# Kernel tuning notes

Hardware: AMD Instinct MI355X
Metric: run time of the kernel (lower is better)

## Reference

```python
import jax, jax.numpy as jnp
import numpy as np

B, HQ, HKV, D, S, MB = 64, 32, 8, 128, 16, 128  # batch, q heads, kv heads, head_dim, block_size, max blocks
SCALE = 0.08838834764831845  # 1/sqrt(128)


def setup_inputs() -> dict:
    key = jax.random.key(0)
    k1, k2, k3, k4 = jax.random.split(key, 4)
    num_blocks = B * MB
    q = jax.random.normal(k1, (B, HQ, D), dtype=jnp.float32)
    k_cache = jax.random.normal(k2, (num_blocks, S, HKV, D), dtype=jnp.float32)
    v_cache = jax.random.normal(k3, (num_blocks, S, HKV, D), dtype=jnp.float32)
    block_tables = jnp.arange(num_blocks, dtype=jnp.int32).reshape(B, MB)
    context_lens = jax.random.randint(k4, (B,), 1, S * MB + 1, dtype=jnp.int32)
    return {"q": q, "k_cache": k_cache, "v_cache": v_cache,
            "block_tables": block_tables, "context_lens": context_lens}


def reference(q, k_cache, v_cache, block_tables, context_lens):
    # Paged GQA decode attention: gather KV blocks per request, masked softmax.
    b, hq, d = q.shape
    s, hkv = k_cache.shape[1], k_cache.shape[2]
    g = hq // hkv
    # gather paged KV: [B, MB, S, HKV, D] -> [B, L, HKV, D]
    k = k_cache[block_tables].reshape(b, -1, hkv, d)
    v = v_cache[block_tables].reshape(b, -1, hkv, d)
    L = k.shape[1]
    qg = (q * SCALE).reshape(b, hkv, g, d)  # group query heads per kv head
    scores = jnp.einsum('bhgd,blhd->bhgl', qg, k)
    valid = jnp.arange(L, dtype=jnp.int32)[None, :] < context_lens[:, None]  # [B, L]
    scores = jnp.where(valid[:, None, None, :], scores, -jnp.inf)
    p = jax.nn.softmax(scores, axis=-1)
    o = jnp.einsum('bhgl,blhd->bhgd', p, v).reshape(b, hq, d)
    return o
```

## Files before the change

kernel.cpp:

```cpp
#include <hip/hip_runtime.h>
#include <cstddef>

#define NB    64
#define NHQ   32
#define NHKV  8
#define HD    128
#define BS    16
#define NMB   128
#define NG    4
#define LMAX  2048
#define QK_SCALE 0.08838834764831845f

__global__ __launch_bounds__(256)
void paged_gqa_decode(const float* __restrict__ q,
                      const float* __restrict__ k_cache,
                      const float* __restrict__ v_cache,
                      const int*   __restrict__ block_tables,
                      const int*   __restrict__ context_lens,
                      float* __restrict__ out)
{
    const int bh   = blockIdx.x;
    const int b    = bh >> 3;
    const int h    = bh & 7;
    const int tid  = threadIdx.x;
    const int team = tid >> 5;
    const int lane = tid & 31;

    __shared__ float s_p[LMAX * 4];
    __shared__ float s_acc[8][NG][HD];
    __shared__ int   s_bt[NMB];
    __shared__ float s_l[NG];

    const int len = context_lens[b];

    for (int i = tid; i < NMB; i += 256) s_bt[i] = block_tables[b * NMB + i];

    const float* qb = q + ((size_t)b * NHQ + (size_t)h * NG) * HD + lane * 4;
    float4 q0 = *(const float4*)(qb);
    float4 q1 = *(const float4*)(qb + HD);
    float4 q2 = *(const float4*)(qb + 2 * HD);
    float4 q3 = *(const float4*)(qb + 3 * HD);
    q0.x *= QK_SCALE; q0.y *= QK_SCALE; q0.z *= QK_SCALE; q0.w *= QK_SCALE;
    q1.x *= QK_SCALE; q1.y *= QK_SCALE; q1.z *= QK_SCALE; q1.w *= QK_SCALE;
    q2.x *= QK_SCALE; q2.y *= QK_SCALE; q2.z *= QK_SCALE; q2.w *= QK_SCALE;
    q3.x *= QK_SCALE; q3.y *= QK_SCALE; q3.z *= QK_SCALE; q3.w *= QK_SCALE;

    __syncthreads();

    const float* kbase = k_cache + (size_t)h * HD + lane * 4;
    const float* vbase = v_cache + (size_t)h * HD + lane * 4;

    auto slot_off = [&](int p) -> size_t {
        return (size_t)(s_bt[p >> 4] * BS + (p & 15)) * (NHKV * HD);
    };

    auto qk_one = [&](int p, float4 k4) {
        float d0 = q0.x * k4.x + q0.y * k4.y + q0.z * k4.z + q0.w * k4.w;
        float d1 = q1.x * k4.x + q1.y * k4.y + q1.z * k4.z + q1.w * k4.w;
        float d2 = q2.x * k4.x + q2.y * k4.y + q2.z * k4.z + q2.w * k4.w;
        float d3 = q3.x * k4.x + q3.y * k4.y + q3.z * k4.z + q3.w * k4.w;
#pragma unroll
        for (int off = 16; off >= 1; off >>= 1) {
            d0 += __shfl_xor(d0, off, 32);
            d1 += __shfl_xor(d1, off, 32);
            d2 += __shfl_xor(d2, off, 32);
            d3 += __shfl_xor(d3, off, 32);
        }
        if (lane == 0) {
            float* sp = s_p + 4 * p;
            sp[0] = d0; sp[1] = d1; sp[2] = d2; sp[3] = d3;
        }
    };

    {
        int p = team;
        for (; p + 24 < len; p += 32) {
            float4 k0 = *(const float4*)(kbase + slot_off(p));
            float4 k1 = *(const float4*)(kbase + slot_off(p + 8));
            float4 k2 = *(const float4*)(kbase + slot_off(p + 16));
            float4 k3 = *(const float4*)(kbase + slot_off(p + 24));
            qk_one(p,      k0);
            qk_one(p + 8,  k1);
            qk_one(p + 16, k2);
            qk_one(p + 24, k3);
        }
        for (; p < len; p += 8) {
            float4 k0 = *(const float4*)(kbase + slot_off(p));
            qk_one(p, k0);
        }
    }
    __syncthreads();

    {
        const int wv = tid >> 6;
        const int wl = tid & 63;
        float m = -INFINITY;
        for (int p = wl; p < len; p += 64) m = fmaxf(m, s_p[4 * p + wv]);
#pragma unroll
        for (int off = 32; off >= 1; off >>= 1) m = fmaxf(m, __shfl_xor(m, off, 64));
        float l = 0.0f;
        for (int p = wl; p < len; p += 64) {
            float e = __expf(s_p[4 * p + wv] - m);
            s_p[4 * p + wv] = e;
            l += e;
        }
#pragma unroll
        for (int off = 32; off >= 1; off >>= 1) l += __shfl_xor(l, off, 64);
        if (wl == 0) s_l[wv] = l;
    }
    __syncthreads();

    float4 a0 = make_float4(0.f, 0.f, 0.f, 0.f);
    float4 a1 = a0, a2 = a0, a3 = a0;

    auto pv_one = [&](int p, float4 v4) {
        const float* sp = s_p + 4 * p;
        float w0 = sp[0], w1 = sp[1], w2 = sp[2], w3 = sp[3];
        a0.x += w0 * v4.x; a0.y += w0 * v4.y; a0.z += w0 * v4.z; a0.w += w0 * v4.w;
        a1.x += w1 * v4.x; a1.y += w1 * v4.y; a1.z += w1 * v4.z; a1.w += w1 * v4.w;
        a2.x += w2 * v4.x; a2.y += w2 * v4.y; a2.z += w2 * v4.z; a2.w += w2 * v4.w;
        a3.x += w3 * v4.x; a3.y += w3 * v4.y; a3.z += w3 * v4.z; a3.w += w3 * v4.w;
    };

    {
        int p = team;
        for (; p + 24 < len; p += 32) {
            float4 v0 = *(const float4*)(vbase + slot_off(p));
            float4 v1 = *(const float4*)(vbase + slot_off(p + 8));
            float4 v2 = *(const float4*)(vbase + slot_off(p + 16));
            float4 v3 = *(const float4*)(vbase + slot_off(p + 24));
            pv_one(p,      v0);
            pv_one(p + 8,  v1);
            pv_one(p + 16, v2);
            pv_one(p + 24, v3);
        }
        for (; p < len; p += 8) {
            float4 v0 = *(const float4*)(vbase + slot_off(p));
            pv_one(p, v0);
        }
    }

    *(float4*)&s_acc[team][0][lane * 4] = a0;
    *(float4*)&s_acc[team][1][lane * 4] = a1;
    *(float4*)&s_acc[team][2][lane * 4] = a2;
    *(float4*)&s_acc[team][3][lane * 4] = a3;
    __syncthreads();

    if (tid < 128) {
        const int j = tid >> 5;
        const int c = (tid & 31) << 2;
        float sx = 0.f, sy = 0.f, sz = 0.f, sw = 0.f;
#pragma unroll
        for (int t = 0; t < 8; ++t) {
            const float* a = &s_acc[t][j][c];
            sx += a[0]; sy += a[1]; sz += a[2]; sw += a[3];
        }
        const float inv = 1.0f / s_l[j];
        float4 o = make_float4(sx * inv, sy * inv, sz * inv, sw * inv);
        *(float4*)(out + ((size_t)b * NHQ + (size_t)h * NG + j) * HD + c) = o;
    }
}

extern "C" void kernel_launch(void* const* d_in, const int* in_sizes, int n_in,
                              void* d_out, int out_size, void* d_ws, size_t ws_size,
                              hipStream_t stream) {
    const float* q            = (const float*)d_in[0];
    const float* k_cache      = (const float*)d_in[1];
    const float* v_cache      = (const float*)d_in[2];
    const int*   block_tables = (const int*)d_in[3];
    const int*   context_lens = (const int*)d_in[4];
    float*       out          = (float*)d_out;

    paged_gqa_decode<<<dim3(NB * NHKV), dim3(256), 0, stream>>>(
        q, k_cache, v_cache, block_tables, context_lens, out);
}
```

Before: 911.9 us.

## Split paged attention into sequence chunks with a separate reduction kernel

Splits each (batch, kv-head) decode into four 512-token chunks, each computed by its own workgroup that writes a partial max, sum and unnormalized output to workspace. A second kernel merges the partials with log-sum-exp rescaling. This raises the number of workgroups from 512 to 2048 to fill the GPU better and shrinks shared memory per block, which allows higher occupancy. It also unrolls the K/V loads to 8 per iteration and replaces the full per-query shuffle reduction with a transposed butterfly, at the cost of an extra launch and workspace traffic.

```diff
diff --git a/kernel.cpp b/kernel.cpp
--- a/kernel.cpp
+++ b/kernel.cpp
@@ -1,39 +1,46 @@
 #include <hip/hip_runtime.h>
 #include <cstddef>
 
-#define NB    64
-#define NHQ   32
-#define NHKV  8
-#define HD    128
-#define BS    16
-#define NMB   128
-#define NG    4
-#define LMAX  2048
+#define NB     64
+#define NHQ    32
+#define NHKV   8
+#define HD     128
+#define BS     16
+#define NMB    128
+#define NG     4
+#define CHUNK  512
+#define NCHUNK 4
 #define QK_SCALE 0.08838834764831845f
-
-__global__ __launch_bounds__(256)
-void paged_gqa_decode(const float* __restrict__ q,
-                      const float* __restrict__ k_cache,
-                      const float* __restrict__ v_cache,
-                      const int*   __restrict__ block_tables,
-                      const int*   __restrict__ context_lens,
-                      float* __restrict__ out)
+#define WS_STRIDE 520
+
+__global__ __launch_bounds__(256, 4)
+void pa_partial(const float* __restrict__ q,
+                const float* __restrict__ k_cache,
+                const float* __restrict__ v_cache,
+                const int*   __restrict__ block_tables,
+                const int*   __restrict__ context_lens,
+                float*       __restrict__ ws)
 {
-    const int bh   = blockIdx.x;
-    const int b    = bh >> 3;
-    const int h    = bh & 7;
+    const int c   = blockIdx.x & (NCHUNK - 1);
+    const int bh  = blockIdx.x >> 2;
+    const int b   = bh >> 3;
+    const int h   = bh & 7;
+    const int len = context_lens[b];
+    const int start = c * CHUNK;
+    if (start >= len) return;
+    const int n = min(len - start, CHUNK);
+
     const int tid  = threadIdx.x;
     const int team = tid >> 5;
     const int lane = tid & 31;
 
-    __shared__ float s_p[LMAX * 4];
-    __shared__ float s_acc[8][NG][HD];
-    __shared__ int   s_bt[NMB];
-    __shared__ float s_l[NG];
-
-    const int len = context_lens[b];
-
-    for (int i = tid; i < NMB; i += 256) s_bt[i] = block_tables[b * NMB + i];
+    __shared__ float smem[8 * NG * HD];
+    __shared__ int   s_bt[CHUNK / BS];
+    __shared__ float s_m[NG], s_l[NG];
+
+    float* s_p = smem;
+
+    if (tid < CHUNK / BS) s_bt[tid] = block_tables[b * NMB + (start >> 4) + tid];
 
     const float* qb = q + ((size_t)b * NHQ + (size_t)h * NG) * HD + lane * 4;
     float4 q0 = *(const float4*)(qb);
@@ -50,43 +57,41 @@
     const float* kbase = k_cache + (size_t)h * HD + lane * 4;
     const float* vbase = v_cache + (size_t)h * HD + lane * 4;
 
-    auto slot_off = [&](int p) -> size_t {
-        return (size_t)(s_bt[p >> 4] * BS + (p & 15)) * (NHKV * HD);
+    auto soff = [&](int p) -> size_t {
+        return ((size_t)s_bt[p >> 4] * BS + (size_t)(p & 15)) * (NHKV * HD);
     };
+
+    const bool l1 = (lane & 1) != 0;
+    const bool l2 = (lane & 2) != 0;
 
     auto qk_one = [&](int p, float4 k4) {
         float d0 = q0.x * k4.x + q0.y * k4.y + q0.z * k4.z + q0.w * k4.w;
         float d1 = q1.x * k4.x + q1.y * k4.y + q1.z * k4.z + q1.w * k4.w;
         float d2 = q2.x * k4.x + q2.y * k4.y + q2.z * k4.z + q2.w * k4.w;
         float d3 = q3.x * k4.x + q3.y * k4.y + q3.z * k4.z + q3.w * k4.w;
-#pragma unroll
-        for (int off = 16; off >= 1; off >>= 1) {
-            d0 += __shfl_xor(d0, off, 32);
-            d1 += __shfl_xor(d1, off, 32);
-            d2 += __shfl_xor(d2, off, 32);
-            d3 += __shfl_xor(d3, off, 32);
-        }
-        if (lane == 0) {
-            float* sp = s_p + 4 * p;
-            sp[0] = d0; sp[1] = d1; sp[2] = d2; sp[3] = d3;
-        }
+        float u  = l1 ? d1 : d0, uw = l1 ? d0 : d1;
+        u += __shfl_xor(uw, 1, 32);
+        float v  = l1 ? d3 : d2, vw = l1 ? d2 : d3;
+        v += __shfl_xor(vw, 1, 32);
+        float x  = l2 ? v : u,  y  = l2 ? u : v;
+        x += __shfl_xor(y, 2, 32);
+        x += __shfl_xor(x, 4, 32);
+        x += __shfl_xor(x, 8, 32);
+        x += __shfl_xor(x, 16, 32);
+        if (lane < 4) s_p[4 * p + lane] = x;
     };
 
     {
         int p = team;
-        for (; p + 24 < len; p += 32) {
-            float4 k0 = *(const float4*)(kbase + slot_off(p));
-            float4 k1 = *(const float4*)(kbase + slot_off(p + 8));
-            float4 k2 = *(const float4*)(kbase + slot_off(p + 16));
-            float4 k3 = *(const float4*)(kbase + slot_off(p + 24));
-            qk_one(p,      k0);
-            qk_one(p + 8,  k1);
-            qk_one(p + 16, k2);
-            qk_one(p + 24, k3);
-        }
-        for (; p < len; p += 8) {
-            float4 k0 = *(const float4*)(kbase + slot_off(p));
-            qk_one(p, k0);
+        for (; p + 56 < n; p += 64) {
+            float4 kk[8];
+#pragma unroll
+            for (int u = 0; u < 8; ++u) kk[u] = *(const float4*)(kbase + soff(p + 8 * u));
+#pragma unroll
+            for (int u = 0; u < 8; ++u) qk_one(p + 8 * u, kk[u]);
+        }
+        for (; p < n; p += 8) {
+            qk_one(p, *(const float4*)(kbase + soff(p)));
         }
     }
     __syncthreads();
@@ -95,18 +100,18 @@
         const int wv = tid >> 6;
         const int wl = tid & 63;
         float m = -INFINITY;
-        for (int p = wl; p < len; p += 64) m = fmaxf(m, s_p[4 * p + wv]);
+        for (int p = wl; p < n; p += 64) m = fmaxf(m, s_p[4 * p + wv]);
 #pragma unroll
         for (int off = 32; off >= 1; off >>= 1) m = fmaxf(m, __shfl_xor(m, off, 64));
         float l = 0.0f;
-        for (int p = wl; p < len; p += 64) {
+        for (int p = wl; p < n; p += 64) {
             float e = __expf(s_p[4 * p + wv] - m);
             s_p[4 * p + wv] = e;
             l += e;
         }
 #pragma unroll
         for (int off = 32; off >= 1; off >>= 1) l += __shfl_xor(l, off, 64);
-        if (wl == 0) s_l[wv] = l;
+        if (wl == 0) { s_m[wv] = m; s_l[wv] = l; }
     }
     __syncthreads();
 
@@ -124,40 +129,64 @@
 
     {
         int p = team;
-        for (; p + 24 < len; p += 32) {
-            float4 v0 = *(const float4*)(vbase + slot_off(p));
-            float4 v1 = *(const float4*)(vbase + slot_off(p + 8));
-            float4 v2 = *(const float4*)(vbase + slot_off(p + 16));
-            float4 v3 = *(const float4*)(vbase + slot_off(p + 24));
-            pv_one(p,      v0);
-            pv_one(p + 8,  v1);
-            pv_one(p + 16, v2);
-            pv_one(p + 24, v3);
-        }
-        for (; p < len; p += 8) {
-            float4 v0 = *(const float4*)(vbase + slot_off(p));
-            pv_one(p, v0);
-        }
-    }
-
+        for (; p + 56 < n; p += 64) {
+            float4 vv[8];
+#pragma unroll
+            for (int u = 0; u < 8; ++u) vv[u] = *(const float4*)(vbase + soff(p + 8 * u));
+#pragma unroll
+            for (int u = 0; u < 8; ++u) pv_one(p + 8 * u, vv[u]);
+        }
+        for (; p < n; p += 8) {
+            pv_one(p, *(const float4*)(vbase + soff(p)));
+        }
+    }
+    __syncthreads();
+
+    float (*s_acc)[NG][HD] = (float (*)[NG][HD])smem;
     *(float4*)&s_acc[team][0][lane * 4] = a0;
     *(float4*)&s_acc[team][1][lane * 4] = a1;
     *(float4*)&s_acc[team][2][lane * 4] = a2;
     *(float4*)&s_acc[team][3][lane * 4] = a3;
     __syncthreads();
 
+    float* wsb = ws + (size_t)(bh * NCHUNK + c) * WS_STRIDE;
     if (tid < 128) {
-        const int j = tid >> 5;
-        const int c = (tid & 31) << 2;
+        const int j  = tid >> 5;
+        const int d4 = (tid & 31) << 2;
         float sx = 0.f, sy = 0.f, sz = 0.f, sw = 0.f;
 #pragma unroll
         for (int t = 0; t < 8; ++t) {
-            const float* a = &s_acc[t][j][c];
+            const float* a = &s_acc[t][j][d4];
             sx += a[0]; sy += a[1]; sz += a[2]; sw += a[3];
         }
-        const float inv = 1.0f / s_l[j];
-        float4 o = make_float4(sx * inv, sy * inv, sz * inv, sw * inv);
-        *(float4*)(out + ((size_t)b * NHQ + (size_t)h * NG + j) * HD + c) = o;
+        *(float4*)(wsb + 8 + j * HD + d4) = make_float4(sx, sy, sz, sw);
+    }
+    if (tid < NG) { wsb[tid] = s_m[tid]; wsb[NG + tid] = s_l[tid]; }
+}
+
+__global__ __launch_bounds__(256)
+void pa_reduce(const int* __restrict__ context_lens,
+               const float* __restrict__ ws,
+               float* __restrict__ out)
+{
+    const int bh  = blockIdx.x;
+    const int b   = bh >> 3;
+    const int h   = bh & 7;
+    const int len = context_lens[b];
+    const int nc  = (len + CHUNK - 1) / CHUNK;
+    const float* base = ws + (size_t)bh * NCHUNK * WS_STRIDE;
+
+    for (int e = threadIdx.x; e < NG * HD; e += 256) {
+        const int j = e >> 7;
+        float m = -INFINITY;
+        for (int cI = 0; cI < nc; ++cI) m = fmaxf(m, base[cI * WS_STRIDE + j]);
+        float acc = 0.f, l = 0.f;
+        for (int cI = 0; cI < nc; ++cI) {
+            const float w = __expf(base[cI * WS_STRIDE + j] - m);
+            l   += w * base[cI * WS_STRIDE + NG + j];
+            acc += w * base[cI * WS_STRIDE + 8 + e];
+        }
+        out[((size_t)b * NHQ + (size_t)h * NG) * HD + e] = acc / l;
     }
 }
 
@@ -170,7 +199,10 @@
     const int*   block_tables = (const int*)d_in[3];
     const int*   context_lens = (const int*)d_in[4];
     float*       out          = (float*)d_out;
-
-    paged_gqa_decode<<<dim3(NB * NHKV), dim3(256), 0, stream>>>(
-        q, k_cache, v_cache, block_tables, context_lens, out);
+    float*       ws           = (float*)d_ws;
+
+    pa_partial<<<dim3(NB * NHKV * NCHUNK), dim3(256), 0, stream>>>(
+        q, k_cache, v_cache, block_tables, context_lens, ws);
+    pa_reduce<<<dim3(NB * NHKV), dim3(256), 0, stream>>>(
+        context_lens, ws, out);
 }
```

Result: no change. 914.5 us (+0.3%).
